# Kernel optimization log

Hardware: AMD Instinct MI355X
Metric: run time of the kernel (lower is better)

The kernel has to match this reference:

```python
import jax, jax.numpy as jnp
import numpy as np

B, T, D, H = 2, 2048, 2048, 16
HD = D // H  # 128


def setup_inputs() -> dict:
    key = jax.random.key(0)
    ks = jax.random.split(key, 9)
    s = 0.02
    return {
        "x": jax.random.normal(ks[0], (B, T, D), jnp.float32),
        "Wq": jax.random.normal(ks[1], (D, D), jnp.float32) * s,
        "bq": jnp.zeros((D,), jnp.float32),
        "Wk": jax.random.normal(ks[2], (D, HD), jnp.float32) * s,
        "bk": jnp.zeros((HD,), jnp.float32),
        "Wv": jax.random.normal(ks[3], (D, HD), jnp.float32) * s,
        "bv": jnp.zeros((HD,), jnp.float32),
        "Wo": jax.random.normal(ks[4], (D, D), jnp.float32) * s,
        "bo": jnp.zeros((D,), jnp.float32),
    }


def reference(x, Wq, bq, Wk, bk, Wv, bv, Wo, bo):
    Bx, Tx, Dx = x.shape
    hd = Wk.shape[1]
    h = Dx // hd
    # Q: (B, T, D) -> (B, H, T, hd)
    q = (x @ Wq + bq).reshape(Bx, Tx, h, hd).transpose(0, 2, 1, 3)
    # K, V: single shared head (B, T, hd) -> (B, 1, T, hd) via broadcast in einsum
    k = x @ Wk + bk  # (B, T, hd)
    v = x @ Wv + bv  # (B, T, hd)
    scale = 1.0 / jnp.sqrt(jnp.asarray(hd, x.dtype))
    # scores: (B, H, Tq, Tk); shared K broadcasts across all H query heads
    scores = jnp.einsum("bhqd,bkd->bhqk", q, k) * scale
    causal = jnp.tril(jnp.ones((Tx, Tx), bool))  # (Tq, Tk)
    scores = jnp.where(causal, scores, jnp.asarray(-1e9, scores.dtype))
    attn = jax.nn.softmax(scores, axis=-1)
    # out: (B, H, Tq, hd) with shared V
    out = jnp.einsum("bhqk,bkd->bhqd", attn, v)
    out = out.transpose(0, 2, 1, 3).reshape(Bx, Tx, Dx)
    return out @ Wo + bo
```

## Files before the change

kernel.cpp:

```cpp
#include <hip/hip_runtime.h>
#include <cstdint>
#include <cstddef>

#define Bq 2
#define Tq 2048
#define Dq 2048
#define Hq 16
#define HDq 128

using f32x4  = __attribute__((ext_vector_type(4))) float;
using short8 = __attribute__((ext_vector_type(8))) short;
typedef unsigned short ushort_t;

#define QSC 0.12751741772f

#define GLOAD_LDS16(gp, lp)                                                        \
  __builtin_amdgcn_global_load_lds((const __attribute__((address_space(1))) void*)(gp), \
                                   (__attribute__((address_space(3))) void*)(lp), 16, 0, 0)

__device__ inline ushort_t f2bf(float f) {
  uint32_t u = __float_as_uint(f);
  uint32_t r = (u + 0x7FFFu + ((u >> 16) & 1u)) >> 16;
  return (ushort_t)r;
}

__device__ inline uint32_t cvt_pk_bf16(float a, float b) {
  uint32_t r;
  asm("v_cvt_pk_bf16_f32 %0, %1, %2" : "=v"(r) : "v"(a), "v"(b));
  return r;
}

__global__ void cast_f32_bf16(const float* __restrict__ in, ushort_t* __restrict__ out, int n4) {
  int stride = gridDim.x * blockDim.x;
  for (int i = blockIdx.x * blockDim.x + threadIdx.x; i < n4; i += stride) {
    float4 v = reinterpret_cast<const float4*>(in)[i];
    ushort4 u;
    u.x = f2bf(v.x); u.y = f2bf(v.y); u.z = f2bf(v.z); u.w = f2bf(v.w);
    reinterpret_cast<ushort4*>(out)[i] = u;
  }
}

__global__ void cast_transpose(const float* __restrict__ in, ushort_t* __restrict__ out,
                               int R, int C, int row_off) {
  __shared__ float tile[32][33];
  int c0 = blockIdx.x * 32, r0 = blockIdx.y * 32;
  int tx = threadIdx.x, ty = threadIdx.y;
#pragma unroll
  for (int i = ty; i < 32; i += 8)
    tile[i][tx] = in[(size_t)(r0 + i) * C + c0 + tx];
  __syncthreads();
#pragma unroll
  for (int i = ty; i < 32; i += 8)
    out[(size_t)(row_off + c0 + i) * R + r0 + tx] = f2bf(tile[tx][i]);
}

template <int OUT_MODE>
__global__ __launch_bounds__(256, 3) void gemm_bt(
    const ushort_t* __restrict__ A, const ushort_t* __restrict__ BT,
    const float* __restrict__ bias, void* __restrict__ Cout,
    int M, int N, int K,
    ushort_t* __restrict__ Kout, ushort_t* __restrict__ VTout,
    const float* __restrict__ bias2, const float* __restrict__ bias3) {
  constexpr int BM = 128, BN = 128, BK = 32;
  __shared__ ushort_t As[BM * BK];
  __shared__ ushort_t Bs[BN * BK];
  const int tid = threadIdx.x;
  const int wave = tid >> 6, lane = tid & 63;
  const int wr = wave >> 1, wc = wave & 1;
  const int m0 = blockIdx.y * BM, n0 = blockIdx.x * BN;
  const int lrow = lane & 15, lk8 = (lane >> 4) * 8;

  f32x4 acc[4][4] = {};

  for (int k0 = 0; k0 < K; k0 += BK) {
#pragma unroll
    for (int p = 0; p < 2; ++p) {
      int byteoff = p * 4096 + wave * 1024;
      int e = (byteoff >> 1) + lane * 8;
      int r = e >> 5, c = e & 31;
      GLOAD_LDS16(A + (size_t)(m0 + r) * K + k0 + c, (char*)As + byteoff);
      GLOAD_LDS16(BT + (size_t)(n0 + r) * K + k0 + c, (char*)Bs + byteoff);
    }
    __syncthreads();
    short8 af[4], bfr[4];
#pragma unroll
    for (int i = 0; i < 4; ++i)
      af[i] = *(const short8*)&As[(wr * 64 + i * 16 + lrow) * BK + lk8];
#pragma unroll
    for (int i = 0; i < 4; ++i)
      bfr[i] = *(const short8*)&Bs[(wc * 64 + i * 16 + lrow) * BK + lk8];
#pragma unroll
    for (int mi = 0; mi < 4; ++mi)
#pragma unroll
      for (int ni = 0; ni < 4; ++ni)
        acc[mi][ni] = __builtin_amdgcn_mfma_f32_16x16x32_bf16(af[mi], bfr[ni], acc[mi][ni], 0, 0, 0);
    __syncthreads();
  }

#pragma unroll
  for (int mi = 0; mi < 4; ++mi) {
#pragma unroll
    for (int ni = 0; ni < 4; ++ni) {
      int rbase = m0 + wr * 64 + mi * 16 + (lane >> 4) * 4;
      int col = n0 + wc * 64 + ni * 16 + lrow;
#pragma unroll
      for (int jj = 0; jj < 4; ++jj) {
        int r = rbase + jj;
        float v = acc[mi][ni][jj];
        if (OUT_MODE == 1) {
          ((float*)Cout)[(size_t)r * N + col] = v + bias[col];
        } else {
          if (col < Dq) {
            ((ushort_t*)Cout)[(size_t)r * Dq + col] = f2bf((v + bias[col]) * QSC);
          } else if (col < Dq + HDq) {
            int d = col - Dq;
            Kout[(size_t)r * HDq + d] = f2bf(v + bias2[d]);
          } else {
            int d = col - Dq - HDq;
            int b = r >> 11, t = r & (Tq - 1);
            VTout[((size_t)b * HDq + d) * Tq + t] = f2bf(v + bias3[d]);
          }
        }
      }
    }
  }
}

__global__ __launch_bounds__(512, 2) void mqa_attn(
    const ushort_t* __restrict__ Qb, const ushort_t* __restrict__ Kb,
    const ushort_t* __restrict__ VTb, ushort_t* __restrict__ Ab) {
  const int bid = blockIdx.x;
  const int g = bid >> 5, bh = bid & 31;
  const int b = bh >> 4, h = bh & 15;
  const int qtA = 15 - g, qtB = g;
  const int ktA = 2 * qtA + 2;
  const int NT = 36;

  const int tid = threadIdx.x;
  const int wave = tid >> 6, lane = tid & 63;
  const int lrow = lane & 15, lk8 = (lane >> 4) * 8;

  __shared__ ushort_t Ks[2][64 * 128];
  __shared__ ushort_t Vs[2][128 * 64];
  __shared__ ushort_t Pl[8][16][76];

  const size_t vtb = (size_t)b * HDq * Tq;
  const size_t kbb = (size_t)b * Tq * HDq;

  size_t kgoff[2], vgoff[2];
#pragma unroll
  for (int rnd = 0; rnd < 2; ++rnd) {
    const int base = rnd * 8192 + wave * 1024;
    const int L = base + lane * 16;
    const int r = L >> 8, c = L & 255;
    kgoff[rnd] = (size_t)r * HDq + ((c ^ ((r & 7) << 4)) >> 1);
    const int r2 = L >> 7, c2 = L & 127;
    vgoff[rnd] = (size_t)r2 * Tq + ((c2 ^ ((r2 & 7) << 4)) >> 1);
  }

  auto stage = [&](int kt, int buf) {
#pragma unroll
    for (int rnd = 0; rnd < 2; ++rnd) {
      const int base = rnd * 8192 + wave * 1024;
      GLOAD_LDS16(Kb + kbb + (size_t)kt * 64 * HDq + kgoff[rnd],
                  (char*)Ks + buf * 16384 + base);
      GLOAD_LDS16(VTb + vtb + kt * 64 + vgoff[rnd],
                  (char*)Vs + buf * 16384 + base);
    }
  };

  short8 qf[4];
  auto loadq = [&](int qtX) {
    const size_t qrow = (size_t)(b * Tq + qtX * 128 + wave * 16 + lrow) * Dq + h * HDq;
#pragma unroll
    for (int dc = 0; dc < 4; ++dc)
      qf[dc] = *(const short8*)(Qb + qrow + dc * 32 + lk8);
  };

  f32x4 o[8] = {};
  float l_run[4] = {0.f, 0.f, 0.f, 0.f};

  auto finalize = [&](int qtX) {
    float inv[4];
#pragma unroll
    for (int jj = 0; jj < 4; ++jj) {
      float l = l_run[jj];
#pragma unroll
      for (int off = 1; off < 16; off <<= 1) l += __shfl_xor(l, off, 64);
      inv[jj] = 1.f / l;
    }
    const size_t orow = (size_t)(b * Tq + qtX * 128 + wave * 16 + (lane >> 4) * 4);
#pragma unroll
    for (int df = 0; df < 8; ++df) {
      const int col = h * HDq + df * 16 + lrow;
#pragma unroll
      for (int jj = 0; jj < 4; ++jj)
        Ab[(orow + jj) * Dq + col] = f2bf(o[df][jj] * inv[jj]);
    }
  };

  loadq(qtA);
  int qt = qtA;

  stage(0, 0);
  __syncthreads();

  int cur = 0;
  for (int s = 0; s < NT; ++s) {
    if (s + 1 < NT) {
      const int sn = s + 1;
      stage(sn < ktA ? sn : sn - ktA, cur ^ 1);
    }
    if (s == ktA) {
      finalize(qtA);
#pragma unroll
      for (int df = 0; df < 8; ++df) o[df] = (f32x4){0.f, 0.f, 0.f, 0.f};
#pragma unroll
      for (int jj = 0; jj < 4; ++jj) l_run[jj] = 0.f;
      loadq(qtB);
      qt = qtB;
    }
    const int kt = (s < ktA) ? s : s - ktA;

    f32x4 sc[4] = {};
#pragma unroll
    for (int ni = 0; ni < 4; ++ni) {
      const int R = ni * 16 + lrow;
#pragma unroll
      for (int dc = 0; dc < 4; ++dc) {
        const int C = (dc * 64 + lk8 * 2) ^ ((R & 7) << 4);
        short8 kf = *(const short8*)((const char*)Ks + cur * 16384 + R * 256 + C);
        sc[ni] = __builtin_amdgcn_mfma_f32_16x16x32_bf16(qf[dc], kf, sc[ni], 0, 0, 0);
      }
    }

    const int qr0 = qt * 128 + wave * 16;
    if (kt * 64 + 63 > qr0) {
      const int qg = qr0 + ((lane >> 4) << 2);
#pragma unroll
      for (int ni = 0; ni < 4; ++ni) {
        const int kg = kt * 64 + ni * 16 + lrow;
#pragma unroll
        for (int jj = 0; jj < 4; ++jj)
          if (kg > qg + jj) sc[ni][jj] = -1e30f;
      }
    }

    const int rb = (lane >> 4) * 4;
#pragma unroll
    for (int ni = 0; ni < 4; ++ni) {
      float p0 = exp2f(fminf(sc[ni][0], 24.f) - 8.f);
      float p1 = exp2f(fminf(sc[ni][1], 24.f) - 8.f);
      float p2 = exp2f(fminf(sc[ni][2], 24.f) - 8.f);
      float p3 = exp2f(fminf(sc[ni][3], 24.f) - 8.f);
      l_run[0] += p0; l_run[1] += p1; l_run[2] += p2; l_run[3] += p3;
      const uint32_t u01 = cvt_pk_bf16(p0, p1);
      const uint32_t u23 = cvt_pk_bf16(p2, p3);
      const int col = ni * 16 + lrow;
      Pl[wave][rb + 0][col] = (ushort_t)u01;
      Pl[wave][rb + 1][col] = (ushort_t)(u01 >> 16);
      Pl[wave][rb + 2][col] = (ushort_t)u23;
      Pl[wave][rb + 3][col] = (ushort_t)(u23 >> 16);
    }

    short8 pa[2];
#pragma unroll
    for (int kc = 0; kc < 2; ++kc)
      pa[kc] = *(const short8*)&Pl[wave][lrow][kc * 32 + lk8];
#pragma unroll
    for (int df = 0; df < 8; ++df) {
      const int R = df * 16 + lrow;
#pragma unroll
      for (int kc = 0; kc < 2; ++kc) {
        const int C = (kc * 64 + lk8 * 2) ^ ((R & 7) << 4);
        short8 vf = *(const short8*)((const char*)Vs + cur * 16384 + R * 128 + C);
        o[df] = __builtin_amdgcn_mfma_f32_16x16x32_bf16(pa[kc], vf, o[df], 0, 0, 0);
      }
    }

    __syncthreads();
    cur ^= 1;
  }

  finalize(qtB);
}

extern "C" void kernel_launch(void* const* d_in, const int* in_sizes, int n_in,
                              void* d_out, int out_size, void* d_ws, size_t ws_size,
                              hipStream_t stream) {
  const float* x  = (const float*)d_in[0];
  const float* Wq = (const float*)d_in[1];
  const float* bq = (const float*)d_in[2];
  const float* Wk = (const float*)d_in[3];
  const float* bk = (const float*)d_in[4];
  const float* Wv = (const float*)d_in[5];
  const float* bv = (const float*)d_in[6];
  const float* Wo = (const float*)d_in[7];
  const float* bo = (const float*)d_in[8];
  float* out = (float*)d_out;

  char* ws = (char*)d_ws;
  ushort_t* xb     = (ushort_t*)(ws);
  ushort_t* WqkvT  = (ushort_t*)(ws + 16777216);
  ushort_t* WoT    = (ushort_t*)(ws + 26214400);
  ushort_t* Qb     = (ushort_t*)(ws + 34603008);
  ushort_t* Kb     = (ushort_t*)(ws + 51380224);
  ushort_t* VTb    = (ushort_t*)(ws + 52428800);
  ushort_t* Ab     = (ushort_t*)(ws + 53477376);

  const int MT = Bq * Tq;

  cast_f32_bf16<<<2048, 256, 0, stream>>>(x, xb, MT * Dq / 4);
  cast_transpose<<<dim3(Dq / 32, Dq / 32), dim3(32, 8), 0, stream>>>(Wq, WqkvT, Dq, Dq, 0);
  cast_transpose<<<dim3(HDq / 32, Dq / 32), dim3(32, 8), 0, stream>>>(Wk, WqkvT, Dq, HDq, 2048);
  cast_transpose<<<dim3(HDq / 32, Dq / 32), dim3(32, 8), 0, stream>>>(Wv, WqkvT, Dq, HDq, 2176);
  cast_transpose<<<dim3(Dq / 32, Dq / 32), dim3(32, 8), 0, stream>>>(Wo, WoT, Dq, Dq, 0);

  gemm_bt<3><<<dim3(2304 / 128, MT / 128), 256, 0, stream>>>(
      xb, WqkvT, bq, Qb, MT, 2304, Dq, Kb, VTb, bk, bv);

  mqa_attn<<<256, 512, 0, stream>>>(Qb, Kb, VTb, Ab);

  gemm_bt<1><<<dim3(Dq / 128, MT / 128), 256, 0, stream>>>(
      Ab, WoT, bo, out, MT, Dq, Dq, nullptr, nullptr, nullptr, nullptr);
}
```

Measured before the change: 224.4 us.

## Restructure MQA attention to 4-wave blocks with two query tiles per wave

The attention kernel now runs 512 blocks of 256 threads, one per (q-tile, head). Before, 256 blocks of 512 threads each paired two q-tiles. Each wave now handles 32 query rows, so every K/V fragment read from LDS feeds two MFMAs, and the P scratch uses an XOR swizzle instead of padding. The GEMMs also switch to a 1D grid with a blockIdx remap so that neighbouring workgroups are spread across XCDs. The risks are more register pressure from doubled accumulators and load imbalance, since each block now does a different amount of causal work.

```diff
diff --git a/kernel.cpp b/kernel.cpp
--- a/kernel.cpp
+++ b/kernel.cpp
@@ -58,7 +58,7 @@
 __global__ __launch_bounds__(256, 3) void gemm_bt(
     const ushort_t* __restrict__ A, const ushort_t* __restrict__ BT,
     const float* __restrict__ bias, void* __restrict__ Cout,
-    int M, int N, int K,
+    int M, int N, int K, int NXT,
     ushort_t* __restrict__ Kout, ushort_t* __restrict__ VTout,
     const float* __restrict__ bias2, const float* __restrict__ bias3) {
   constexpr int BM = 128, BN = 128, BK = 32;
@@ -67,7 +67,9 @@
   const int tid = threadIdx.x;
   const int wave = tid >> 6, lane = tid & 63;
   const int wr = wave >> 1, wc = wave & 1;
-  const int m0 = blockIdx.y * BM, n0 = blockIdx.x * BN;
+  const int nwg = gridDim.x;
+  const int orig = (blockIdx.x & 7) * (nwg >> 3) + (blockIdx.x >> 3);
+  const int m0 = (orig / NXT) * BM, n0 = (orig % NXT) * BN;
   const int lrow = lane & 15, lk8 = (lane >> 4) * 8;
 
   f32x4 acc[4][4] = {};
@@ -126,31 +128,30 @@
   }
 }
 
-__global__ __launch_bounds__(512, 2) void mqa_attn(
+__global__ __launch_bounds__(256, 2) void mqa_attn(
     const ushort_t* __restrict__ Qb, const ushort_t* __restrict__ Kb,
     const ushort_t* __restrict__ VTb, ushort_t* __restrict__ Ab) {
   const int bid = blockIdx.x;
-  const int g = bid >> 5, bh = bid & 31;
+  const int bh = bid & 31;
   const int b = bh >> 4, h = bh & 15;
-  const int qtA = 15 - g, qtB = g;
-  const int ktA = 2 * qtA + 2;
-  const int NT = 36;
-
-  const int tid = threadIdx.x;
-  const int wave = tid >> 6, lane = tid & 63;
+  const int qt = (bid < 256) ? (15 - (bid >> 5)) : ((bid - 256) >> 5);
+  const int NT = 2 * qt + 2;
+
+  const int wave = threadIdx.x >> 6, lane = threadIdx.x & 63;
   const int lrow = lane & 15, lk8 = (lane >> 4) * 8;
+  const int rb = (lane >> 4) * 4;
 
   __shared__ ushort_t Ks[2][64 * 128];
   __shared__ ushort_t Vs[2][128 * 64];
-  __shared__ ushort_t Pl[8][16][76];
+  __shared__ ushort_t Pl[4][32 * 64];
 
   const size_t vtb = (size_t)b * HDq * Tq;
   const size_t kbb = (size_t)b * Tq * HDq;
 
-  size_t kgoff[2], vgoff[2];
-#pragma unroll
-  for (int rnd = 0; rnd < 2; ++rnd) {
-    const int base = rnd * 8192 + wave * 1024;
+  size_t kgoff[4], vgoff[4];
+#pragma unroll
+  for (int rnd = 0; rnd < 4; ++rnd) {
+    const int base = rnd * 4096 + wave * 1024;
     const int L = base + lane * 16;
     const int r = L >> 8, c = L & 255;
     kgoff[rnd] = (size_t)r * HDq + ((c ^ ((r & 7) << 4)) >> 1);
@@ -160,8 +161,8 @@
 
   auto stage = [&](int kt, int buf) {
 #pragma unroll
-    for (int rnd = 0; rnd < 2; ++rnd) {
-      const int base = rnd * 8192 + wave * 1024;
+    for (int rnd = 0; rnd < 4; ++rnd) {
+      const int base = rnd * 4096 + wave * 1024;
       GLOAD_LDS16(Kb + kbb + (size_t)kt * 64 * HDq + kgoff[rnd],
                   (char*)Ks + buf * 16384 + base);
       GLOAD_LDS16(VTb + vtb + kt * 64 + vgoff[rnd],
@@ -169,104 +170,86 @@
     }
   };
 
-  short8 qf[4];
-  auto loadq = [&](int qtX) {
-    const size_t qrow = (size_t)(b * Tq + qtX * 128 + wave * 16 + lrow) * Dq + h * HDq;
+  short8 qf[2][4];
+#pragma unroll
+  for (int mi = 0; mi < 2; ++mi) {
+    const size_t qrow = (size_t)(b * Tq + qt * 128 + wave * 32 + mi * 16 + lrow) * Dq + h * HDq;
 #pragma unroll
     for (int dc = 0; dc < 4; ++dc)
-      qf[dc] = *(const short8*)(Qb + qrow + dc * 32 + lk8);
-  };
-
-  f32x4 o[8] = {};
-  float l_run[4] = {0.f, 0.f, 0.f, 0.f};
-
-  auto finalize = [&](int qtX) {
-    float inv[4];
-#pragma unroll
-    for (int jj = 0; jj < 4; ++jj) {
-      float l = l_run[jj];
-#pragma unroll
-      for (int off = 1; off < 16; off <<= 1) l += __shfl_xor(l, off, 64);
-      inv[jj] = 1.f / l;
-    }
-    const size_t orow = (size_t)(b * Tq + qtX * 128 + wave * 16 + (lane >> 4) * 4);
-#pragma unroll
-    for (int df = 0; df < 8; ++df) {
-      const int col = h * HDq + df * 16 + lrow;
-#pragma unroll
-      for (int jj = 0; jj < 4; ++jj)
-        Ab[(orow + jj) * Dq + col] = f2bf(o[df][jj] * inv[jj]);
-    }
-  };
-
-  loadq(qtA);
-  int qt = qtA;
+      qf[mi][dc] = *(const short8*)(Qb + qrow + dc * 32 + lk8);
+  }
+
+  f32x4 o[2][8] = {};
+  float l_run[2][4] = {};
 
   stage(0, 0);
   __syncthreads();
 
   int cur = 0;
   for (int s = 0; s < NT; ++s) {
-    if (s + 1 < NT) {
-      const int sn = s + 1;
-      stage(sn < ktA ? sn : sn - ktA, cur ^ 1);
-    }
-    if (s == ktA) {
-      finalize(qtA);
-#pragma unroll
-      for (int df = 0; df < 8; ++df) o[df] = (f32x4){0.f, 0.f, 0.f, 0.f};
-#pragma unroll
-      for (int jj = 0; jj < 4; ++jj) l_run[jj] = 0.f;
-      loadq(qtB);
-      qt = qtB;
-    }
-    const int kt = (s < ktA) ? s : s - ktA;
-
-    f32x4 sc[4] = {};
+    if (s + 1 < NT) stage(s + 1, cur ^ 1);
+    const int kt = s;
+
+    f32x4 sc[2][4] = {};
 #pragma unroll
     for (int ni = 0; ni < 4; ++ni) {
       const int R = ni * 16 + lrow;
+      short8 kf[4];
 #pragma unroll
       for (int dc = 0; dc < 4; ++dc) {
         const int C = (dc * 64 + lk8 * 2) ^ ((R & 7) << 4);
-        short8 kf = *(const short8*)((const char*)Ks + cur * 16384 + R * 256 + C);
-        sc[ni] = __builtin_amdgcn_mfma_f32_16x16x32_bf16(qf[dc], kf, sc[ni], 0, 0, 0);
-      }
-    }
-
-    const int qr0 = qt * 128 + wave * 16;
-    if (kt * 64 + 63 > qr0) {
-      const int qg = qr0 + ((lane >> 4) << 2);
+        kf[dc] = *(const short8*)((const char*)Ks + cur * 16384 + R * 256 + C);
+      }
+#pragma unroll
+      for (int dc = 0; dc < 4; ++dc) {
+        sc[0][ni] = __builtin_amdgcn_mfma_f32_16x16x32_bf16(qf[0][dc], kf[dc], sc[0][ni], 0, 0, 0);
+        sc[1][ni] = __builtin_amdgcn_mfma_f32_16x16x32_bf16(qf[1][dc], kf[dc], sc[1][ni], 0, 0, 0);
+      }
+    }
+
+#pragma unroll
+    for (int mi = 0; mi < 2; ++mi) {
+      const int qr0 = qt * 128 + wave * 32 + mi * 16;
+      if (kt * 64 + 63 > qr0) {
+        const int qg = qr0 + rb;
+#pragma unroll
+        for (int ni = 0; ni < 4; ++ni) {
+          const int kg = kt * 64 + ni * 16 + lrow;
+#pragma unroll
+          for (int jj = 0; jj < 4; ++jj)
+            if (kg > qg + jj) sc[mi][ni][jj] = -1e30f;
+        }
+      }
+    }
+
+#pragma unroll
+    for (int mi = 0; mi < 2; ++mi) {
 #pragma unroll
       for (int ni = 0; ni < 4; ++ni) {
-        const int kg = kt * 64 + ni * 16 + lrow;
-#pragma unroll
-        for (int jj = 0; jj < 4; ++jj)
-          if (kg > qg + jj) sc[ni][jj] = -1e30f;
-      }
-    }
-
-    const int rb = (lane >> 4) * 4;
-#pragma unroll
-    for (int ni = 0; ni < 4; ++ni) {
-      float p0 = exp2f(fminf(sc[ni][0], 24.f) - 8.f);
-      float p1 = exp2f(fminf(sc[ni][1], 24.f) - 8.f);
-      float p2 = exp2f(fminf(sc[ni][2], 24.f) - 8.f);
-      float p3 = exp2f(fminf(sc[ni][3], 24.f) - 8.f);
-      l_run[0] += p0; l_run[1] += p1; l_run[2] += p2; l_run[3] += p3;
-      const uint32_t u01 = cvt_pk_bf16(p0, p1);
-      const uint32_t u23 = cvt_pk_bf16(p2, p3);
-      const int col = ni * 16 + lrow;
-      Pl[wave][rb + 0][col] = (ushort_t)u01;
-      Pl[wave][rb + 1][col] = (ushort_t)(u01 >> 16);
-      Pl[wave][rb + 2][col] = (ushort_t)u23;
-      Pl[wave][rb + 3][col] = (ushort_t)(u23 >> 16);
-    }
-
-    short8 pa[2];
-#pragma unroll
-    for (int kc = 0; kc < 2; ++kc)
-      pa[kc] = *(const short8*)&Pl[wave][lrow][kc * 32 + lk8];
+        float p0 = exp2f(fminf(sc[mi][ni][0], 24.f) - 8.f);
+        float p1 = exp2f(fminf(sc[mi][ni][1], 24.f) - 8.f);
+        float p2 = exp2f(fminf(sc[mi][ni][2], 24.f) - 8.f);
+        float p3 = exp2f(fminf(sc[mi][ni][3], 24.f) - 8.f);
+        l_run[mi][0] += p0; l_run[mi][1] += p1;
+        l_run[mi][2] += p2; l_run[mi][3] += p3;
+        const uint32_t u01 = cvt_pk_bf16(p0, p1);
+        const uint32_t u23 = cvt_pk_bf16(p2, p3);
+        const int col = ni * 16 + lrow;
+        const int rowb = mi * 16 + rb;
+        Pl[wave][(rowb + 0) * 64 + (col ^ ((rb << 2) ^ 0))]  = (ushort_t)u01;
+        Pl[wave][(rowb + 1) * 64 + (col ^ ((rb << 2) ^ 8))]  = (ushort_t)(u01 >> 16);
+        Pl[wave][(rowb + 2) * 64 + (col ^ ((rb << 2) ^ 16))] = (ushort_t)u23;
+        Pl[wave][(rowb + 3) * 64 + (col ^ ((rb << 2) ^ 24))] = (ushort_t)(u23 >> 16);
+      }
+    }
+
+    short8 pa[2][2];
+    const int fsw = ((lrow & 12) << 2) ^ ((lrow & 3) << 3);
+#pragma unroll
+    for (int mi = 0; mi < 2; ++mi)
+#pragma unroll
+      for (int kc = 0; kc < 2; ++kc)
+        pa[mi][kc] = *(const short8*)&Pl[wave][(mi * 16 + lrow) * 64 + ((kc * 32 + lk8) ^ fsw)];
 #pragma unroll
     for (int df = 0; df < 8; ++df) {
       const int R = df * 16 + lrow;
@@ -274,7 +257,8 @@
       for (int kc = 0; kc < 2; ++kc) {
         const int C = (kc * 64 + lk8 * 2) ^ ((R & 7) << 4);
         short8 vf = *(const short8*)((const char*)Vs + cur * 16384 + R * 128 + C);
-        o[df] = __builtin_amdgcn_mfma_f32_16x16x32_bf16(pa[kc], vf, o[df], 0, 0, 0);
+        o[0][df] = __builtin_amdgcn_mfma_f32_16x16x32_bf16(pa[0][kc], vf, o[0][df], 0, 0, 0);
+        o[1][df] = __builtin_amdgcn_mfma_f32_16x16x32_bf16(pa[1][kc], vf, o[1][df], 0, 0, 0);
       }
     }
 
@@ -282,7 +266,25 @@
     cur ^= 1;
   }
 
-  finalize(qtB);
+#pragma unroll
+  for (int mi = 0; mi < 2; ++mi) {
+    float inv[4];
+#pragma unroll
+    for (int jj = 0; jj < 4; ++jj) {
+      float l = l_run[mi][jj];
+#pragma unroll
+      for (int off = 1; off < 16; off <<= 1) l += __shfl_xor(l, off, 64);
+      inv[jj] = 1.f / l;
+    }
+    const size_t orow = (size_t)(b * Tq + qt * 128 + wave * 32 + mi * 16 + rb);
+#pragma unroll
+    for (int df = 0; df < 8; ++df) {
+      const int col = h * HDq + df * 16 + lrow;
+#pragma unroll
+      for (int jj = 0; jj < 4; ++jj)
+        Ab[(orow + jj) * Dq + col] = f2bf(o[mi][df][jj] * inv[jj]);
+    }
+  }
 }
 
 extern "C" void kernel_launch(void* const* d_in, const int* in_sizes, int n_in,
@@ -316,11 +318,11 @@
   cast_transpose<<<dim3(HDq / 32, Dq / 32), dim3(32, 8), 0, stream>>>(Wv, WqkvT, Dq, HDq, 2176);
   cast_transpose<<<dim3(Dq / 32, Dq / 32), dim3(32, 8), 0, stream>>>(Wo, WoT, Dq, Dq, 0);
 
-  gemm_bt<3><<<dim3(2304 / 128, MT / 128), 256, 0, stream>>>(
-      xb, WqkvT, bq, Qb, MT, 2304, Dq, Kb, VTb, bk, bv);
-
-  mqa_attn<<<256, 512, 0, stream>>>(Qb, Kb, VTb, Ab);
-
-  gemm_bt<1><<<dim3(Dq / 128, MT / 128), 256, 0, stream>>>(
-      Ab, WoT, bo, out, MT, Dq, Dq, nullptr, nullptr, nullptr, nullptr);
-}
+  gemm_bt<3><<<(2304 / 128) * (MT / 128), 256, 0, stream>>>(
+      xb, WqkvT, bq, Qb, MT, 2304, Dq, 2304 / 128, Kb, VTb, bk, bv);
+
+  mqa_attn<<<512, 256, 0, stream>>>(Qb, Kb, VTb, Ab);
+
+  gemm_bt<1><<<(Dq / 128) * (MT / 128), 256, 0, stream>>>(
+      Ab, WoT, bo, out, MT, Dq, Dq, Dq / 128, nullptr, nullptr, nullptr, nullptr);
+}
```

After: 218.6 us. 1.03x faster.
